# Kernel tuning notes

Hardware: AMD Instinct MI355X
Metric: run time of the kernel (lower is better)

## Reference

```python
import jax, jax.numpy as jnp
import numpy as np

INPUT_DIM = 362
HIDDEN = 256
STYLE_NUM = 60
OUTFIT_NUM = 49710
BATCH = 16384


def setup_inputs() -> dict:
    key = jax.random.key(0)
    ks = jax.random.split(key, 12)
    f32 = jnp.float32
    return {
        "i_feature": jax.random.normal(ks[0], (BATCH, INPUT_DIM), f32),
        "j_feature": jax.random.normal(ks[1], (BATCH, INPUT_DIM), f32),
        "k_feature": jax.random.normal(ks[2], (BATCH, INPUT_DIM), f32),
        # top_emb / bottom_emb Linear params (stored transposed: x @ W + b)
        "W_top": jax.random.normal(ks[3], (INPUT_DIM, HIDDEN), f32) * 0.05,
        "b_top": jnp.zeros((HIDDEN,), f32),
        "W_bot": jax.random.normal(ks[4], (INPUT_DIM, HIDDEN), f32) * 0.05,
        "b_bot": jnp.zeros((HIDDEN,), f32),
        # NMF factors (forward relu_'s them in place; we relu on use)
        "P_nmf": jax.random.normal(ks[5], (2 * INPUT_DIM, STYLE_NUM), f32),
        "N_nmf": jax.random.normal(ks[6], (2 * INPUT_DIM, STYLE_NUM), f32),
        "H1_nmf": jax.random.normal(ks[7], (STYLE_NUM, OUTFIT_NUM), f32),
        "H2_nmf": jax.random.normal(ks[8], (STYLE_NUM, OUTFIT_NUM), f32),
        "matirx_pos": jax.random.uniform(ks[9], (2 * INPUT_DIM, OUTFIT_NUM), f32),
        "matirx_neg": jax.random.uniform(ks[10], (2 * INPUT_DIM, OUTFIT_NUM), f32),
    }


def _emb(x, W, b):
    # nn.Sequential(Linear, Sigmoid)
    return jax.nn.sigmoid(x @ W + b)


def _style_score(i_f, j_f, styles, W_top, b_top, W_bot, b_bot):
    # Vectorized version of the per-sample loop:
    # squared-distance argmin codebook lookup + gather + rowwise dot.
    outfit = jnp.concatenate([i_f, j_f], axis=1)  # [B, 2D]
    # mean over feature dim of (x - s)^2; constant 1/(2D) scale does not change argmin
    d2 = (jnp.sum(outfit * outfit, axis=1, keepdims=True)
          - 2.0 * (outfit @ styles)
          + jnp.sum(styles * styles, axis=0, keepdims=True))  # [B, S]
    idx = jnp.argmin(d2, axis=1)                               # [B]
    sel = styles.T[idx]                                        # [B, 2D] gather
    top, bot = sel[:, :INPUT_DIM], sel[:, INPUT_DIM:]
    # diag(matmul) == rowwise dot
    return jnp.sum(_emb(top, W_top, b_top) * _emb(bot, W_bot, b_bot), axis=1)  # [B]


def reference(i_feature, j_feature, k_feature, W_top, b_top, W_bot, b_bot,
              P_nmf, N_nmf, H1_nmf, H2_nmf, matirx_pos, matirx_neg):
    Ti = _emb(i_feature, W_top, b_top)   # [B, H]
    Bj = _emb(j_feature, W_bot, b_bot)   # [B, H]
    Bk = _emb(k_feature, W_bot, b_bot)   # [B, H]
    # torch.diag(matmul(Ti, Bj.T)) == rowwise dot (avoids [B,B] intermediate)
    ij_score = jnp.sum(Ti * Bj, axis=1)  # [B]
    ik_score = jnp.sum(Ti * Bk, axis=1)  # [B]

    # forward does relu_ on .data before use
    P = jnp.maximum(P_nmf, 0.0)
    N = jnp.maximum(N_nmf, 0.0)
    H1 = jnp.maximum(H1_nmf, 0.0)
    H2 = jnp.maximum(H2_nmf, 0.0)

    style_ij = _style_score(i_feature, j_feature, P, W_top, b_top, W_bot, b_bot)
    style_ik = _style_score(i_feature, k_feature, N, W_top, b_top, W_bot, b_bot)

    # -mean(log(sigmoid(d))) computed stably
    loss1 = -jnp.mean(jax.nn.log_sigmoid(ij_score - ik_score))
    loss2 = -jnp.mean(jax.nn.log_sigmoid(style_ij - style_ik))
    loss3 = jnp.mean(jnp.square(matirx_pos - P @ H1)
                     + jnp.square(matirx_neg - N @ H2))
    loss = loss1 + loss2 + 0.1 * loss3

    ij_ik = jnp.stack([ij_score, ik_score], axis=1)  # [B, 2]
    auc = jnp.mean((jnp.argmax(ij_ik, axis=1) == 0).astype(jnp.float32))
    return (loss, loss1, loss2, loss3, auc)
```

## Files before the change

### kernel.cpp

```cpp
#include <hip/hip_runtime.h>
#include <math.h>

#define BATCH 16384
#define IND   362
#define KP    384
#define HID   256
#define STY   60
#define NOUT  49710
#define OUTP  49920
#define D2    724
#define D2P   768

#define NB_HR   3120
#define NB_CW   768
#define NB_CPN  384
#define NB_CF   9216
#define NB_CONV (NB_HR + NB_CW + NB_CPN + NB_CF)

#define NB_SS   120

#define OCH     256
#define N_OC    195
#define DHALF   368
#define NTILES  23
#define NB_M    (2 * 2 * N_OC)

#define NB_EMB  1024
#define NB_SA   512
#define NB_HH   16
#define NB_PPB  2
#define NB_HEAD (NB_HH + NB_PPB)

typedef __bf16 bf16x8 __attribute__((ext_vector_type(8)));
typedef float  floatx4 __attribute__((ext_vector_type(4)));
typedef float  floatx2 __attribute__((ext_vector_type(2)));

__device__ inline floatx4 mfma16(bf16x8 a, bf16x8 b, floatx4 c) {
  return __builtin_amdgcn_mfma_f32_16x16x32_bf16(a, b, c, 0, 0, 0);
}

__device__ inline unsigned short f32_to_bf16(float x) {
  unsigned int u = __float_as_uint(x);
  unsigned int r = (u + 0x7FFFu + ((u >> 16) & 1u)) >> 16;
  return (unsigned short)r;
}

__device__ inline float sigm_fast(float x) { return 1.0f / (1.0f + __expf(-x)); }
__device__ inline float softplusf(float z) { return fmaxf(z, 0.0f) + log1pf(expf(-fabsf(z))); }

__global__ __launch_bounds__(256) void k_conv(
    const float* __restrict__ fi, const float* __restrict__ fj, const float* __restrict__ fk,
    const float* __restrict__ Wt, const float* __restrict__ Wb,
    const float* __restrict__ Pn, const float* __restrict__ Nn,
    const float* __restrict__ H1, const float* __restrict__ H2,
    unsigned short* __restrict__ fbf, unsigned short* __restrict__ wbfT,
    unsigned short* __restrict__ pnbfT, unsigned short* __restrict__ hrows,
    float* __restrict__ Pr) {
  int b = blockIdx.x;
  int t = threadIdx.x;

  if (b < NB_HR) {
    int e = (b * 256 + t) * 8;
    int row = e / OUTP;
    int o = e - row * OUTP;
    int s = row & 63;
    int mm = row >> 6;
    const float* H = mm ? H2 : H1;
    unsigned short* dst = hrows + (size_t)row * OUTP + o;
    unsigned int wv[4];
    if (s < STY && o + 8 <= NOUT) {
      const float* src = H + (size_t)s * NOUT + o;
      #pragma unroll
      for (int ee = 0; ee < 4; ee++) {
        floatx2 v = *(const floatx2*)(src + 2 * ee);
        wv[ee] = (unsigned)f32_to_bf16(fmaxf(v[0], 0.0f)) |
                 ((unsigned)f32_to_bf16(fmaxf(v[1], 0.0f)) << 16);
      }
    } else {
      #pragma unroll
      for (int ee = 0; ee < 4; ee++) {
        float lo = (s < STY && o + 2 * ee     < NOUT) ? fmaxf(H[(size_t)s * NOUT + o + 2 * ee],     0.0f) : 0.0f;
        float hi = (s < STY && o + 2 * ee + 1 < NOUT) ? fmaxf(H[(size_t)s * NOUT + o + 2 * ee + 1], 0.0f) : 0.0f;
        wv[ee] = (unsigned)f32_to_bf16(lo) | ((unsigned)f32_to_bf16(hi) << 16);
      }
    }
    uint4 v; v.x = wv[0]; v.y = wv[1]; v.z = wv[2]; v.w = wv[3];
    *(uint4*)dst = v;
    return;
  }
  b -= NB_HR;

  if (b < NB_CW) {
    int idx = b * 256 + t;
    int k = idx % KP;
    int rem = idx / KP;
    int h = rem % HID;
    int mm = rem / HID;
    const float* W = mm ? Wb : Wt;
    wbfT[idx] = f32_to_bf16(k < IND ? W[(size_t)k * HID + h] : 0.0f);
    return;
  }
  b -= NB_CW;

  if (b < NB_CPN) {
    int u = b * 256 + t;
    int s = u & 63;
    int v = u >> 6;
    int m = (v >= D2P) ? 1 : 0;
    int d = v - m * D2P;
    const float* M = m ? Nn : Pn;
    float x = (d < D2 && s < STY) ? fmaxf(M[(size_t)d * STY + s], 0.0f) : 0.0f;
    unsigned short bb = f32_to_bf16(x);
    int k = (d < IND) ? d : (d < D2 ? d + 22 : (d < 746 ? d - IND : d));
    pnbfT[((size_t)m * 64 + s) * D2P + k] = bb;
    Pr[((size_t)m * D2P + d) * 64 + s] = x;
    return;
  }
  b -= NB_CPN;

  {
    long u = (long)b * 256 + t;
    int g = (int)(u % 48);
    long rf = u / 48;
    int row = (int)(rf % BATCH);
    int f = (int)(rf / BATCH);
    const float* src = (f == 0) ? fi : (f == 1 ? fj : fk);
    int d0 = g * 8;
    const float* sp = src + (size_t)row * IND + d0;
    unsigned int wv[4];
    #pragma unroll
    for (int e = 0; e < 4; e++) {
      int dd = d0 + 2 * e;
      float lo = (dd < IND)     ? sp[2 * e]     : 0.0f;
      float hi = (dd + 1 < IND) ? sp[2 * e + 1] : 0.0f;
      wv[e] = (unsigned)f32_to_bf16(lo) | ((unsigned)f32_to_bf16(hi) << 16);
    }
    uint4 v; v.x = wv[0]; v.y = wv[1]; v.z = wv[2]; v.w = wv[3];
    *(uint4*)(fbf + ((size_t)f * BATCH + row) * KP + d0) = v;
  }
}

__global__ __launch_bounds__(256) void k_style(
    const float* __restrict__ Wt, const float* __restrict__ btop,
    const float* __restrict__ Wb, const float* __restrict__ bbot,
    const float* __restrict__ Pn, const float* __restrict__ Nn,
    float* __restrict__ ss, float* __restrict__ cn) {
  __shared__ float sel[D2];
  __shared__ float shr[4];
  int b = blockIdx.x;
  int t = threadIdx.x;
  int s  = b % STY;
  int mt = b / STY;
  const float* M = mt ? Nn : Pn;
  float cnp = 0.0f;
  for (int d = t; d < D2; d += 256) {
    float v = fmaxf(M[(size_t)d * STY + s], 0.0f);
    sel[d] = v;
    cnp += v * v;
  }
  __syncthreads();
  float at = btop[t], ab = bbot[t];
  for (int d = 0; d < IND; d++) at = fmaf(sel[d],       Wt[(size_t)d * HID + t], at);
  for (int d = 0; d < IND; d++) ab = fmaf(sel[IND + d], Wb[(size_t)d * HID + t], ab);
  float prod = (1.0f / (1.0f + expf(-at))) * (1.0f / (1.0f + expf(-ab)));
  for (int off = 32; off > 0; off >>= 1) prod += __shfl_xor(prod, off);
  if ((t & 63) == 0) shr[t >> 6] = prod;
  __syncthreads();
  if (t == 0) ss[mt * 64 + s] = shr[0] + shr[1] + shr[2] + shr[3];
  __syncthreads();
  for (int off = 32; off > 0; off >>= 1) cnp += __shfl_xor(cnp, off);
  if ((t & 63) == 0) shr[t >> 6] = cnp;
  __syncthreads();
  if (t == 0) cn[mt * 64 + s] = shr[0] + shr[1] + shr[2] + shr[3];
}

__global__ __launch_bounds__(256) void k_m(
    const unsigned short* __restrict__ hrows, const float* __restrict__ Pr,
    const float* __restrict__ mp, const float* __restrict__ mneg,
    float* __restrict__ partial) {
  __shared__ unsigned short Hs[64 * OCH];
  __shared__ float red[4];
  int w = threadIdx.x >> 6, lane = threadIdx.x & 63;
  int m = lane & 15, q = lane >> 4;

  int b = blockIdx.x;
  int oc  = b % N_OC;
  int r   = b / N_OC;
  int dh  = r & 1;
  int mat = r >> 1;
  int o0 = oc * OCH;
  bool full = (o0 + OCH <= NOUT);
  const float* Mbase = mat ? mneg : mp;
  const float* Prb   = Pr + (size_t)mat * D2P * 64;

  char* HsB = (char*)Hs;
  #pragma unroll
  for (int rr = 0; rr < 16; rr++) {
    int R = w * 16 + rr;
    uint2 hv = *(const uint2*)(hrows + ((size_t)mat * 64 + R) * OUTP + o0 + lane * 4);
    *(uint2*)(HsB + R * 512 + ((lane * 8) ^ ((R & 7) << 4))) = hv;
  }
  __syncthreads();

  int xm = (m & 7) << 4;
  float msq = 0.0f, t2 = 0.0f;
  floatx2 mreg[32];
  floatx4 preg[4];

  auto ISSUE_M = [&](int t) {
    int d = dh * DHALF + t * 16 + m;
    bool ok = (d < D2);
    const float* Mr = Mbase + (size_t)d * NOUT + o0 + q * 8;
    if (ok && full) {
      #pragma unroll
      for (int kc = 0; kc < 8; kc++) {
        mreg[kc * 4 + 0] = *(const floatx2*)(Mr + kc * 32);
        mreg[kc * 4 + 1] = *(const floatx2*)(Mr + kc * 32 + 2);
        mreg[kc * 4 + 2] = *(const floatx2*)(Mr + kc * 32 + 4);
        mreg[kc * 4 + 3] = *(const floatx2*)(Mr + kc * 32 + 6);
      }
    } else {
      #pragma unroll
      for (int kc = 0; kc < 8; kc++) {
        #pragma unroll
        for (int e = 0; e < 4; e++) {
          int o = o0 + kc * 32 + q * 8 + 2 * e;
          floatx2 v = {0.f, 0.f};
          if (ok) {
            if (o     < NOUT) v[0] = Mbase[(size_t)d * NOUT + o];
            if (o + 1 < NOUT) v[1] = Mbase[(size_t)d * NOUT + o + 1];
          }
          mreg[kc * 4 + e] = v;
        }
      }
    }
  };
  auto ISSUE_P = [&](int t) {
    int d = dh * DHALF + t * 16 + m;
    const float* Pp = Prb + (size_t)d * 64 + q * 4;
    #pragma unroll
    for (int st = 0; st < 4; st++) preg[st] = *(const floatx4*)(Pp + st * 16);
  };

  int t0 = w;
  if (t0 < NTILES) { ISSUE_M(t0); ISSUE_P(t0); }
  for (int t = t0; t < NTILES; t += 4) {
    bf16x8 bf[8];
    #pragma unroll
    for (int kc = 0; kc < 8; kc++) {
      union { unsigned int u[4]; bf16x8 v; } cv;
      #pragma unroll
      for (int e = 0; e < 4; e++) {
        floatx2 tv = mreg[kc * 4 + e];
        msq = fmaf(tv[0], tv[0], msq);
        msq = fmaf(tv[1], tv[1], msq);
        cv.u[e] = (unsigned)f32_to_bf16(tv[0]) | ((unsigned)f32_to_bf16(tv[1]) << 16);
      }
      bf[kc] = cv.v;
    }
    int tn = t + 4;
    if (tn < NTILES) ISSUE_M(tn);

    floatx4 acc[4];
    #pragma unroll
    for (int st = 0; st < 4; st++) acc[st] = (floatx4){0.f, 0.f, 0.f, 0.f};
    #pragma unroll
    for (int kc = 0; kc < 8; kc++) {
      #pragma unroll
      for (int st = 0; st < 4; st++) {
        bf16x8 hf = *(const bf16x8*)(HsB + (st * 16 + m) * 512 + ((kc * 64 + q * 16) ^ xm));
        acc[st] = mfma16(hf, bf[kc], acc[st]);
      }
    }

    #pragma unroll
    for (int st = 0; st < 4; st++)
      #pragma unroll
      for (int rg = 0; rg < 4; rg++)
        t2 = fmaf(preg[st][rg], acc[st][rg], t2);
    if (tn < NTILES) ISSUE_P(tn);
  }

  float local = msq - 2.0f * t2;
  for (int off = 32; off > 0; off >>= 1) local += __shfl_xor(local, off);
  if (lane == 0) red[w] = local;
  __syncthreads();
  if (threadIdx.x == 0) partial[blockIdx.x] = red[0] + red[1] + red[2] + red[3];
}

__global__ __launch_bounds__(256, 4) void k_emb(
    const unsigned short* __restrict__ fbf, const unsigned short* __restrict__ wbfT,
    const float* __restrict__ btop, const float* __restrict__ bbot,
    float* __restrict__ sIJ, float* __restrict__ sIK) {
  int w = threadIdx.x >> 6, lane = threadIdx.x & 63;
  int m = lane & 15, q = lane >> 4;
  int b = blockIdx.x;
  int r0 = (b & 255) * 64 + w * 16;
  int hb = (b >> 8) * 64;
  const unsigned short* fi = fbf + (size_t)(r0 + m) * KP + q * 8;
  const unsigned short* fj = fi + (size_t)BATCH * KP;
  const unsigned short* fk = fj + (size_t)BATCH * KP;
  floatx4 accI[4], accJ[4], accK[4];
  #pragma unroll
  for (int nt = 0; nt < 4; nt++) {
    accI[nt] = (floatx4){0.f, 0.f, 0.f, 0.f};
    accJ[nt] = (floatx4){0.f, 0.f, 0.f, 0.f};
    accK[nt] = (floatx4){0.f, 0.f, 0.f, 0.f};
  }
  for (int kc = 0; kc < 12; kc++) {
    bf16x8 ai = *(const bf16x8*)(fi + kc * 32);
    bf16x8 aj = *(const bf16x8*)(fj + kc * 32);
    bf16x8 ak = *(const bf16x8*)(fk + kc * 32);
    #pragma unroll
    for (int nt = 0; nt < 4; nt++) {
      int n = hb + nt * 16 + m;
      const unsigned short* wp = wbfT + (size_t)n * KP + kc * 32 + q * 8;
      bf16x8 bt8 = *(const bf16x8*)(wp);
      bf16x8 bb8 = *(const bf16x8*)(wp + (size_t)HID * KP);
      accI[nt] = mfma16(ai, bt8, accI[nt]);
      accJ[nt] = mfma16(aj, bb8, accJ[nt]);
      accK[nt] = mfma16(ak, bb8, accK[nt]);
    }
  }
  float sij[4] = {0.f, 0.f, 0.f, 0.f}, sik[4] = {0.f, 0.f, 0.f, 0.f};
  #pragma unroll
  for (int nt = 0; nt < 4; nt++) {
    int n = hb + nt * 16 + m;
    float vbt = btop[n], vbb = bbot[n];
    #pragma unroll
    for (int reg = 0; reg < 4; reg++) {
      float ti = sigm_fast(accI[nt][reg] + vbt);
      float tj = sigm_fast(accJ[nt][reg] + vbb);
      float tk = sigm_fast(accK[nt][reg] + vbb);
      sij[reg] += ti * tj;
      sik[reg] += ti * tk;
    }
  }
  #pragma unroll
  for (int reg = 0; reg < 4; reg++) {
    for (int off = 1; off < 16; off <<= 1) {
      sij[reg] += __shfl_xor(sij[reg], off);
      sik[reg] += __shfl_xor(sik[reg], off);
    }
  }
  if (m == 0) {
    #pragma unroll
    for (int reg = 0; reg < 4; reg++) {
      int row = r0 + q * 4 + reg;
      atomicAdd(&sIJ[row], sij[reg]);
      atomicAdd(&sIK[row], sik[reg]);
    }
  }
}

__global__ __launch_bounds__(256, 4) void k_sa(
    const unsigned short* __restrict__ fbf, const unsigned short* __restrict__ pnbfT,
    const float* __restrict__ cn, const float* __restrict__ ss,
    float* __restrict__ stIJ, float* __restrict__ stIK) {
  int w = threadIdx.x >> 6, lane = threadIdx.x & 63;
  int m = lane & 15, q = lane >> 4;
  int b = blockIdx.x;
  int mat = w & 1;
  int r0 = b * 32 + (w >> 1) * 16;
  const unsigned short* fA = fbf + (size_t)(r0 + m) * KP + q * 8;
  const unsigned short* fB = fA + (size_t)(1 + mat) * BATCH * KP;
  const unsigned short* Bp = pnbfT + (size_t)mat * 64 * D2P + q * 8;
  floatx4 acc[4];
  #pragma unroll
  for (int nt = 0; nt < 4; nt++) acc[nt] = (floatx4){0.f, 0.f, 0.f, 0.f};
  for (int kc = 0; kc < 24; kc++) {
    bf16x8 a = (kc < 12) ? *(const bf16x8*)(fA + kc * 32)
                         : *(const bf16x8*)(fB + (kc - 12) * 32);
    #pragma unroll
    for (int nt = 0; nt < 4; nt++) {
      bf16x8 bb = *(const bf16x8*)(Bp + (size_t)(nt * 16 + m) * D2P + kc * 32);
      acc[nt] = mfma16(a, bb, acc[nt]);
    }
  }
  const float* cnm = cn + mat * 64;
  float bv[4]; int bi[4];
  #pragma unroll
  for (int reg = 0; reg < 4; reg++) { bv[reg] = __builtin_inff(); bi[reg] = 1 << 30; }
  #pragma unroll
  for (int nt = 0; nt < 4; nt++) {
    int s = nt * 16 + m;
    float c = cnm[s & 63];
    #pragma unroll
    for (int reg = 0; reg < 4; reg++) {
      float d2 = (s < STY) ? (c - 2.0f * acc[nt][reg]) : __builtin_inff();
      if (d2 < bv[reg] || (d2 == bv[reg] && s < bi[reg])) { bv[reg] = d2; bi[reg] = s; }
    }
  }
  for (int off = 1; off < 16; off <<= 1) {
    #pragma unroll
    for (int reg = 0; reg < 4; reg++) {
      float ov = __shfl_xor(bv[reg], off);
      int   oi = __shfl_xor(bi[reg], off);
      if (ov < bv[reg] || (ov == bv[reg] && oi < bi[reg])) { bv[reg] = ov; bi[reg] = oi; }
    }
  }
  if (m == 0) {
    float* dst = mat ? stIK : stIJ;
    const float* ssm = ss + mat * 64;
    #pragma unroll
    for (int reg = 0; reg < 4; reg++) dst[r0 + q * 4 + reg] = ssm[bi[reg]];
  }
}

__global__ __launch_bounds__(256) void k_head(
    const unsigned short* __restrict__ pnbfT, const unsigned short* __restrict__ hrows,
    float* __restrict__ HHb, float* __restrict__ PPb) {
  __shared__ float red[4096];
  int w = threadIdx.x >> 6, lane = threadIdx.x & 63;
  int m = lane & 15, q = lane >> 4;
  int b = blockIdx.x;
  bool isPP = (b >= NB_HH);
  int mat, chunk, nsteps, stride;
  const unsigned short* Rb;
  if (!isPP) { mat = b >> 3; chunk = b & 7; Rb = hrows + (size_t)mat * 64 * OUTP; stride = OUTP; nsteps = 195; }
  else       { mat = b - NB_HH; chunk = 0; Rb = pnbfT + (size_t)mat * 64 * D2P;  stride = D2P;  nsteps = 24;  }
  const unsigned short* Rm = Rb + (size_t)m * stride;

  floatx4 acc[4][4];
  #pragma unroll
  for (int a2 = 0; a2 < 4; a2++)
    #pragma unroll
    for (int b2 = 0; b2 < 4; b2++) acc[a2][b2] = (floatx4){0.f, 0.f, 0.f, 0.f};

  bf16x8 hc[4], hn[4];
  auto LD = [&](int j, bf16x8* hh) {
    int k = (chunk * nsteps + j) * 32 + q * 8;
    #pragma unroll
    for (int st = 0; st < 4; st++)
      hh[st] = *(const bf16x8*)(Rm + (size_t)(st * 16) * stride + k);
  };
  int j = w;
  LD(j, hc);
  for (; j < nsteps; j += 4) {
    if (j + 4 < nsteps) LD(j + 4, hn);
    #pragma unroll
    for (int a2 = 0; a2 < 4; a2++)
      #pragma unroll
      for (int b2 = 0; b2 < 4; b2++)
        acc[a2][b2] = mfma16(hc[a2], hc[b2], acc[a2][b2]);
    #pragma unroll
    for (int st = 0; st < 4; st++) hc[st] = hn[st];
  }
  for (int idx = threadIdx.x; idx < 4096; idx += 256) red[idx] = 0.f;
  __syncthreads();
  #pragma unroll
  for (int a2 = 0; a2 < 4; a2++)
    #pragma unroll
    for (int b2 = 0; b2 < 4; b2++)
      #pragma unroll
      for (int r = 0; r < 4; r++)
        atomicAdd(&red[(a2 * 16 + q * 4 + r) * 64 + b2 * 16 + m], acc[a2][b2][r]);
  __syncthreads();
  float* dst = (isPP ? PPb : HHb) + (size_t)mat * 4096;
  for (int idx = threadIdx.x; idx < 4096; idx += 256) atomicAdd(&dst[idx], red[idx]);
}

__global__ __launch_bounds__(256) void k_final(
    const float* __restrict__ sIJ, const float* __restrict__ sIK,
    const float* __restrict__ stIJ, const float* __restrict__ stIK,
    const float* __restrict__ l3partial,
    const float* __restrict__ HHb, const float* __restrict__ PPb,
    float* __restrict__ out) {
  int t = threadIdx.x;
  float l1 = 0.f, l2 = 0.f, ac = 0.f;
  for (int r = t; r < BATCH; r += 256) {
    float dij = sIJ[r] - sIK[r];
    l1 += softplusf(-dij);
    if (dij >= 0.0f) ac += 1.0f;
    float dst = stIJ[r] - stIK[r];
    l2 += softplusf(-dst);
  }
  double l3 = 0.0;
  for (int p = t; p < NB_M; p += 256) l3 += (double)l3partial[p];
  for (int idx = t; idx < 8192; idx += 256) l3 += (double)HHb[idx] * (double)PPb[idx];
  __shared__ float sh1[4], sh2[4], sh3[4];
  __shared__ double sh4[4];
  for (int off = 32; off > 0; off >>= 1) {
    l1 += __shfl_xor(l1, off);
    l2 += __shfl_xor(l2, off);
    ac += __shfl_xor(ac, off);
    l3 += __shfl_xor(l3, off);
  }
  if ((t & 63) == 0) { sh1[t >> 6] = l1; sh2[t >> 6] = l2; sh3[t >> 6] = ac; sh4[t >> 6] = l3; }
  __syncthreads();
  if (t == 0) {
    double L1 = 0, L2 = 0, AC = 0, L3 = 0;
    for (int i = 0; i < 4; i++) { L1 += sh1[i]; L2 += sh2[i]; AC += sh3[i]; L3 += sh4[i]; }
    L1 /= BATCH; L2 /= BATCH; AC /= BATCH;
    L3 /= ((double)D2 * (double)NOUT);
    out[0] = (float)(L1 + L2 + 0.1 * L3);
    out[1] = (float)L1;
    out[2] = (float)L2;
    out[3] = (float)L3;
    out[4] = (float)AC;
  }
}

extern "C" void kernel_launch(void* const* d_in, const int* in_sizes, int n_in,
                              void* d_out, int out_size, void* d_ws, size_t ws_size,
                              hipStream_t stream) {
  (void)in_sizes; (void)n_in; (void)out_size; (void)ws_size;
  const float* i_f  = (const float*)d_in[0];
  const float* j_f  = (const float*)d_in[1];
  const float* k_f  = (const float*)d_in[2];
  const float* W_t  = (const float*)d_in[3];
  const float* b_t  = (const float*)d_in[4];
  const float* W_b  = (const float*)d_in[5];
  const float* b_b  = (const float*)d_in[6];
  const float* P_n  = (const float*)d_in[7];
  const float* N_n  = (const float*)d_in[8];
  const float* H1   = (const float*)d_in[9];
  const float* H2   = (const float*)d_in[10];
  const float* Mp   = (const float*)d_in[11];
  const float* Mn   = (const float*)d_in[12];
  float* out = (float*)d_out;
  char* ws = (char*)d_ws;

  const size_t OFF_FBF   = 0;
  const size_t OFF_WBFT  = OFF_FBF   + (size_t)3 * BATCH * KP * 2;
  const size_t OFF_PNBFT = OFF_WBFT  + (size_t)2 * HID * KP * 2;
  const size_t OFF_PR    = OFF_PNBFT + (size_t)2 * 64 * D2P * 2;
  const size_t OFF_HROWS = OFF_PR    + (size_t)2 * D2P * 64 * 4;
  const size_t OFF_SIJ   = OFF_HROWS + (size_t)2 * 64 * OUTP * 2;
  const size_t OFF_SIK   = OFF_SIJ   + (size_t)BATCH * 4;
  const size_t OFF_HH    = OFF_SIK   + (size_t)BATCH * 4;
  const size_t OFF_PP    = OFF_HH    + (size_t)2 * 4096 * 4;
  const size_t OFF_STIJ  = OFF_PP    + (size_t)2 * 4096 * 4;
  const size_t OFF_STIK  = OFF_STIJ  + (size_t)BATCH * 4;
  const size_t OFF_SS    = OFF_STIK  + (size_t)BATCH * 4;
  const size_t OFF_CN    = OFF_SS    + 512;
  const size_t OFF_L3P   = OFF_CN    + 512;

  unsigned short* fbf   = (unsigned short*)(ws + OFF_FBF);
  unsigned short* wbfT  = (unsigned short*)(ws + OFF_WBFT);
  unsigned short* pnbfT = (unsigned short*)(ws + OFF_PNBFT);
  float*          Pr    = (float*)(ws + OFF_PR);
  unsigned short* hrows = (unsigned short*)(ws + OFF_HROWS);
  float*  sIJ  = (float*)(ws + OFF_SIJ);
  float*  sIK  = (float*)(ws + OFF_SIK);
  float*  HHb  = (float*)(ws + OFF_HH);
  float*  PPb  = (float*)(ws + OFF_PP);
  float*  stIJ = (float*)(ws + OFF_STIJ);
  float*  stIK = (float*)(ws + OFF_STIK);
  float*  ss   = (float*)(ws + OFF_SS);
  float*  cn   = (float*)(ws + OFF_CN);
  float*  l3p  = (float*)(ws + OFF_L3P);

  hipMemsetAsync(ws + OFF_SIJ, 0, (size_t)BATCH * 4 * 2 + (size_t)4 * 4096 * 4, stream);

  k_conv<<<NB_CONV, 256, 0, stream>>>(i_f, j_f, k_f, W_t, W_b, P_n, N_n, H1, H2,
                                      fbf, wbfT, pnbfT, hrows, Pr);
  k_style<<<NB_SS, 256, 0, stream>>>(W_t, b_t, W_b, b_b, P_n, N_n, ss, cn);
  k_m<<<NB_M, 256, 0, stream>>>(hrows, Pr, Mp, Mn, l3p);
  k_emb<<<NB_EMB, 256, 0, stream>>>(fbf, wbfT, b_t, b_b, sIJ, sIK);
  k_sa<<<NB_SA, 256, 0, stream>>>(fbf, pnbfT, cn, ss, stIJ, stIK);
  k_head<<<NB_HEAD, 256, 0, stream>>>(pnbfT, hrows, HHb, PPb);
  k_final<<<1, 256, 0, stream>>>(sIJ, sIK, stIJ, stIK, l3p, HHb, PPb, out);
}
```

Baseline: 698.6 us.

## Fuse M, embedding, style-assign and head kernels into one launch; restage M tiles via LDS

Merges the four independent compute kernels (NMF residual, embedding scores, style argmin, Gram heads) into a single block-dispatched kernel, so their work can overlap on the GPU and fewer launches are needed. The NMF residual path is rewritten to load matrix rows coalesced into registers, convert them to bf16 into double-buffered swizzled shared memory, and run one MFMA chain per wave, with a barrier each tile. The final reduction is split into a 64-block partial kernel plus a small finalize kernel, and index arithmetic in the conversion kernel moves from 64-bit to 32-bit. The fused kernel now reserves about 48KB of shared memory for every block, which can lower occupancy for the embedding and style-assign blocks that previously used none.

```diff
diff --git a/kernel.cpp b/kernel.cpp
--- a/kernel.cpp
+++ b/kernel.cpp
@@ -22,14 +22,14 @@
 #define OCH     256
 #define N_OC    195
 #define DHALF   368
-#define NTILES  23
-#define NB_M    (2 * 2 * N_OC)
-
+#define MTILES  23
+#define NB_MB   (2 * 2 * N_OC)
 #define NB_EMB  1024
 #define NB_SA   512
 #define NB_HH   16
 #define NB_PPB  2
 #define NB_HEAD (NB_HH + NB_PPB)
+#define NB_MAIN (NB_MB + NB_EMB + NB_SA + NB_HEAD)
 
 typedef __bf16 bf16x8 __attribute__((ext_vector_type(8)));
 typedef float  floatx4 __attribute__((ext_vector_type(4)));
@@ -119,11 +119,11 @@
   b -= NB_CPN;
 
   {
-    long u = (long)b * 256 + t;
-    int g = (int)(u % 48);
-    long rf = u / 48;
-    int row = (int)(rf % BATCH);
-    int f = (int)(rf / BATCH);
+    int u = b * 256 + t;
+    int g = u % 48;
+    int rf = u / 48;
+    int row = rf % BATCH;
+    int f = rf / BATCH;
     const float* src = (f == 0) ? fi : (f == 1 ? fj : fk);
     int d0 = g * 8;
     const float* sp = src + (size_t)row * IND + d0;
@@ -174,309 +174,301 @@
   if (t == 0) cn[mt * 64 + s] = shr[0] + shr[1] + shr[2] + shr[3];
 }
 
-__global__ __launch_bounds__(256) void k_m(
-    const unsigned short* __restrict__ hrows, const float* __restrict__ Pr,
+__global__ __launch_bounds__(256) void k_main(
+    const unsigned short* __restrict__ fbf, const unsigned short* __restrict__ wbfT,
+    const unsigned short* __restrict__ pnbfT, const unsigned short* __restrict__ hrows,
+    const float* __restrict__ Pr,
+    const float* __restrict__ btop, const float* __restrict__ bbot,
+    const float* __restrict__ cn, const float* __restrict__ ss,
     const float* __restrict__ mp, const float* __restrict__ mneg,
+    float* __restrict__ sIJ, float* __restrict__ sIK,
+    float* __restrict__ stIJ, float* __restrict__ stIK,
+    float* __restrict__ HHb, float* __restrict__ PPb,
     float* __restrict__ partial) {
-  __shared__ unsigned short Hs[64 * OCH];
-  __shared__ float red[4];
-  int w = threadIdx.x >> 6, lane = threadIdx.x & 63;
-  int m = lane & 15, q = lane >> 4;
-
-  int b = blockIdx.x;
-  int oc  = b % N_OC;
-  int r   = b / N_OC;
-  int dh  = r & 1;
-  int mat = r >> 1;
-  int o0 = oc * OCH;
-  bool full = (o0 + OCH <= NOUT);
-  const float* Mbase = mat ? mneg : mp;
-  const float* Prb   = Pr + (size_t)mat * D2P * 64;
-
-  char* HsB = (char*)Hs;
-  #pragma unroll
-  for (int rr = 0; rr < 16; rr++) {
-    int R = w * 16 + rr;
-    uint2 hv = *(const uint2*)(hrows + ((size_t)mat * 64 + R) * OUTP + o0 + lane * 4);
-    *(uint2*)(HsB + R * 512 + ((lane * 8) ^ ((R & 7) << 4))) = hv;
-  }
-  __syncthreads();
-
-  int xm = (m & 7) << 4;
-  float msq = 0.0f, t2 = 0.0f;
-  floatx2 mreg[32];
-  floatx4 preg[4];
-
-  auto ISSUE_M = [&](int t) {
-    int d = dh * DHALF + t * 16 + m;
-    bool ok = (d < D2);
-    const float* Mr = Mbase + (size_t)d * NOUT + o0 + q * 8;
-    if (ok && full) {
-      #pragma unroll
-      for (int kc = 0; kc < 8; kc++) {
-        mreg[kc * 4 + 0] = *(const floatx2*)(Mr + kc * 32);
-        mreg[kc * 4 + 1] = *(const floatx2*)(Mr + kc * 32 + 2);
-        mreg[kc * 4 + 2] = *(const floatx2*)(Mr + kc * 32 + 4);
-        mreg[kc * 4 + 3] = *(const floatx2*)(Mr + kc * 32 + 6);
-      }
-    } else {
-      #pragma unroll
-      for (int kc = 0; kc < 8; kc++) {
-        #pragma unroll
-        for (int e = 0; e < 4; e++) {
-          int o = o0 + kc * 32 + q * 8 + 2 * e;
-          floatx2 v = {0.f, 0.f};
-          if (ok) {
-            if (o     < NOUT) v[0] = Mbase[(size_t)d * NOUT + o];
-            if (o + 1 < NOUT) v[1] = Mbase[(size_t)d * NOUT + o + 1];
-          }
-          mreg[kc * 4 + e] = v;
-        }
-      }
-    }
-  };
-  auto ISSUE_P = [&](int t) {
-    int d = dh * DHALF + t * 16 + m;
-    const float* Pp = Prb + (size_t)d * 64 + q * 4;
-    #pragma unroll
-    for (int st = 0; st < 4; st++) preg[st] = *(const floatx4*)(Pp + st * 16);
-  };
-
-  int t0 = w;
-  if (t0 < NTILES) { ISSUE_M(t0); ISSUE_P(t0); }
-  for (int t = t0; t < NTILES; t += 4) {
-    bf16x8 bf[8];
-    #pragma unroll
-    for (int kc = 0; kc < 8; kc++) {
-      union { unsigned int u[4]; bf16x8 v; } cv;
-      #pragma unroll
-      for (int e = 0; e < 4; e++) {
-        floatx2 tv = mreg[kc * 4 + e];
-        msq = fmaf(tv[0], tv[0], msq);
-        msq = fmaf(tv[1], tv[1], msq);
-        cv.u[e] = (unsigned)f32_to_bf16(tv[0]) | ((unsigned)f32_to_bf16(tv[1]) << 16);
-      }
-      bf[kc] = cv.v;
-    }
-    int tn = t + 4;
-    if (tn < NTILES) ISSUE_M(tn);
-
-    floatx4 acc[4];
-    #pragma unroll
-    for (int st = 0; st < 4; st++) acc[st] = (floatx4){0.f, 0.f, 0.f, 0.f};
-    #pragma unroll
-    for (int kc = 0; kc < 8; kc++) {
-      #pragma unroll
-      for (int st = 0; st < 4; st++) {
-        bf16x8 hf = *(const bf16x8*)(HsB + (st * 16 + m) * 512 + ((kc * 64 + q * 16) ^ xm));
-        acc[st] = mfma16(hf, bf[kc], acc[st]);
-      }
-    }
-
-    #pragma unroll
-    for (int st = 0; st < 4; st++)
-      #pragma unroll
-      for (int rg = 0; rg < 4; rg++)
-        t2 = fmaf(preg[st][rg], acc[st][rg], t2);
-    if (tn < NTILES) ISSUE_P(tn);
-  }
-
-  float local = msq - 2.0f * t2;
-  for (int off = 32; off > 0; off >>= 1) local += __shfl_xor(local, off);
-  if (lane == 0) red[w] = local;
-  __syncthreads();
-  if (threadIdx.x == 0) partial[blockIdx.x] = red[0] + red[1] + red[2] + red[3];
-}
-
-__global__ __launch_bounds__(256, 4) void k_emb(
-    const unsigned short* __restrict__ fbf, const unsigned short* __restrict__ wbfT,
-    const float* __restrict__ btop, const float* __restrict__ bbot,
-    float* __restrict__ sIJ, float* __restrict__ sIK) {
+  __shared__ __align__(16) char smem[49168];
   int w = threadIdx.x >> 6, lane = threadIdx.x & 63;
   int m = lane & 15, q = lane >> 4;
   int b = blockIdx.x;
-  int r0 = (b & 255) * 64 + w * 16;
-  int hb = (b >> 8) * 64;
-  const unsigned short* fi = fbf + (size_t)(r0 + m) * KP + q * 8;
-  const unsigned short* fj = fi + (size_t)BATCH * KP;
-  const unsigned short* fk = fj + (size_t)BATCH * KP;
-  floatx4 accI[4], accJ[4], accK[4];
-  #pragma unroll
-  for (int nt = 0; nt < 4; nt++) {
-    accI[nt] = (floatx4){0.f, 0.f, 0.f, 0.f};
-    accJ[nt] = (floatx4){0.f, 0.f, 0.f, 0.f};
-    accK[nt] = (floatx4){0.f, 0.f, 0.f, 0.f};
-  }
-  for (int kc = 0; kc < 12; kc++) {
-    bf16x8 ai = *(const bf16x8*)(fi + kc * 32);
-    bf16x8 aj = *(const bf16x8*)(fj + kc * 32);
-    bf16x8 ak = *(const bf16x8*)(fk + kc * 32);
+
+  if (b < NB_MB) {
+    int oc  = b % N_OC;
+    int r   = b / N_OC;
+    int dh  = r & 1;
+    int mat = r >> 1;
+    int o0 = oc * OCH;
+    int nvalid = NOUT - o0; if (nvalid > OCH) nvalid = OCH;
+    const float* Mbase = mat ? mneg : mp;
+    const float* Prb   = Pr + (size_t)mat * D2P * 64;
+    char* HsB = smem;
+    char* MsB = smem + 32768;
+    float* shp = (float*)(smem + 49152);
+
+    #pragma unroll
+    for (int rr = 0; rr < 16; rr++) {
+      int R = w * 16 + rr;
+      uint2 hv = *(const uint2*)(hrows + ((size_t)mat * 64 + R) * OUTP + o0 + lane * 4);
+      *(uint2*)(HsB + R * 512 + ((lane * 8) ^ ((R & 7) << 4))) = hv;
+    }
+
+    float msq = 0.0f, t2 = 0.0f;
+    float rgA[4][4], rgB[4][4];
+
+    auto ISSUE = [&](int t, float rg[4][4]) {
+      #pragma unroll
+      for (int rr = 0; rr < 4; rr++) {
+        int row = w * 4 + rr;
+        int d = dh * DHALF + t * 16 + row;
+        bool ok = (d < D2);
+        const float* src = Mbase + (size_t)d * NOUT + o0;
+        #pragma unroll
+        for (int e = 0; e < 4; e++) {
+          int c = lane + 64 * e;
+          rg[rr][e] = (ok && c < nvalid) ? src[c] : 0.0f;
+        }
+      }
+    };
+    auto WRITE = [&](int t, float rg[4][4]) {
+      char* buf = MsB + (t & 1) * 8192;
+      #pragma unroll
+      for (int rr = 0; rr < 4; rr++) {
+        int row = w * 4 + rr;
+        int swz = (row & 7) << 4;
+        #pragma unroll
+        for (int e = 0; e < 4; e++) {
+          float v = rg[rr][e];
+          msq = fmaf(v, v, msq);
+          *(unsigned short*)(buf + row * 512 + (((lane + 64 * e) * 2) ^ swz)) = f32_to_bf16(v);
+        }
+      }
+    };
+
+    ISSUE(0, rgA);
+    ISSUE(1, rgB);
+    WRITE(0, rgA);
+    __syncthreads();
+
+    int xm = (m & 7) << 4;
+    for (int t = 0; t < MTILES; t++) {
+      if (t + 2 < MTILES) ISSUE(t + 2, (t & 1) ? rgB : rgA);
+      int dbase = dh * DHALF + t * 16;
+      floatx4 pv = *(const floatx4*)(Prb + (size_t)(dbase + m) * 64 + w * 16 + q * 4);
+      const char* buf = MsB + (t & 1) * 8192;
+      floatx4 acc = (floatx4){0.f, 0.f, 0.f, 0.f};
+      #pragma unroll
+      for (int kc = 0; kc < 8; kc++) {
+        bf16x8 hf = *(const bf16x8*)(HsB + (w * 16 + m) * 512 + ((kc * 64 + q * 16) ^ xm));
+        bf16x8 mf = *(const bf16x8*)(buf + m * 512 + ((kc * 64 + q * 16) ^ xm));
+        acc = mfma16(hf, mf, acc);
+      }
+      if (t + 1 < MTILES) WRITE(t + 1, (t & 1) ? rgA : rgB);
+      t2 = fmaf(pv[0], acc[0], fmaf(pv[1], acc[1], fmaf(pv[2], acc[2], fmaf(pv[3], acc[3], t2))));
+      __syncthreads();
+    }
+
+    float local = msq - 2.0f * t2;
+    for (int off = 32; off > 0; off >>= 1) local += __shfl_xor(local, off);
+    if (lane == 0) shp[w] = local;
+    __syncthreads();
+    if (threadIdx.x == 0) partial[blockIdx.x] = shp[0] + shp[1] + shp[2] + shp[3];
+    return;
+  }
+  b -= NB_MB;
+
+  if (b < NB_EMB) {
+    int r0 = (b & 255) * 64 + w * 16;
+    int hb = (b >> 8) * 64;
+    const unsigned short* fi = fbf + (size_t)(r0 + m) * KP + q * 8;
+    const unsigned short* fj = fi + (size_t)BATCH * KP;
+    const unsigned short* fk = fj + (size_t)BATCH * KP;
+    floatx4 accI[4], accJ[4], accK[4];
+    #pragma unroll
+    for (int nt = 0; nt < 4; nt++) {
+      accI[nt] = (floatx4){0.f, 0.f, 0.f, 0.f};
+      accJ[nt] = (floatx4){0.f, 0.f, 0.f, 0.f};
+      accK[nt] = (floatx4){0.f, 0.f, 0.f, 0.f};
+    }
+    for (int kc = 0; kc < 12; kc++) {
+      bf16x8 ai = *(const bf16x8*)(fi + kc * 32);
+      bf16x8 aj = *(const bf16x8*)(fj + kc * 32);
+      bf16x8 ak = *(const bf16x8*)(fk + kc * 32);
+      #pragma unroll
+      for (int nt = 0; nt < 4; nt++) {
+        int n = hb + nt * 16 + m;
+        const unsigned short* wp = wbfT + (size_t)n * KP + kc * 32 + q * 8;
+        bf16x8 bt8 = *(const bf16x8*)(wp);
+        bf16x8 bb8 = *(const bf16x8*)(wp + (size_t)HID * KP);
+        accI[nt] = mfma16(ai, bt8, accI[nt]);
+        accJ[nt] = mfma16(aj, bb8, accJ[nt]);
+        accK[nt] = mfma16(ak, bb8, accK[nt]);
+      }
+    }
+    float sij[4] = {0.f, 0.f, 0.f, 0.f}, sik[4] = {0.f, 0.f, 0.f, 0.f};
     #pragma unroll
     for (int nt = 0; nt < 4; nt++) {
       int n = hb + nt * 16 + m;
-      const unsigned short* wp = wbfT + (size_t)n * KP + kc * 32 + q * 8;
-      bf16x8 bt8 = *(const bf16x8*)(wp);
-      bf16x8 bb8 = *(const bf16x8*)(wp + (size_t)HID * KP);
-      accI[nt] = mfma16(ai, bt8, accI[nt]);
-      accJ[nt] = mfma16(aj, bb8, accJ[nt]);
-      accK[nt] = mfma16(ak, bb8, accK[nt]);
-    }
-  }
-  float sij[4] = {0.f, 0.f, 0.f, 0.f}, sik[4] = {0.f, 0.f, 0.f, 0.f};
-  #pragma unroll
-  for (int nt = 0; nt < 4; nt++) {
-    int n = hb + nt * 16 + m;
-    float vbt = btop[n], vbb = bbot[n];
+      float vbt = btop[n], vbb = bbot[n];
+      #pragma unroll
+      for (int reg = 0; reg < 4; reg++) {
+        float ti = sigm_fast(accI[nt][reg] + vbt);
+        float tj = sigm_fast(accJ[nt][reg] + vbb);
+        float tk = sigm_fast(accK[nt][reg] + vbb);
+        sij[reg] += ti * tj;
+        sik[reg] += ti * tk;
+      }
+    }
     #pragma unroll
     for (int reg = 0; reg < 4; reg++) {
-      float ti = sigm_fast(accI[nt][reg] + vbt);
-      float tj = sigm_fast(accJ[nt][reg] + vbb);
-      float tk = sigm_fast(accK[nt][reg] + vbb);
-      sij[reg] += ti * tj;
-      sik[reg] += ti * tk;
-    }
-  }
-  #pragma unroll
-  for (int reg = 0; reg < 4; reg++) {
+      for (int off = 1; off < 16; off <<= 1) {
+        sij[reg] += __shfl_xor(sij[reg], off);
+        sik[reg] += __shfl_xor(sik[reg], off);
+      }
+    }
+    if (m == 0) {
+      #pragma unroll
+      for (int reg = 0; reg < 4; reg++) {
+        int row = r0 + q * 4 + reg;
+        atomicAdd(&sIJ[row], sij[reg]);
+        atomicAdd(&sIK[row], sik[reg]);
+      }
+    }
+    return;
+  }
+  b -= NB_EMB;
+
+  if (b < NB_SA) {
+    int mat = w & 1;
+    int r0 = b * 32 + (w >> 1) * 16;
+    const unsigned short* fA = fbf + (size_t)(r0 + m) * KP + q * 8;
+    const unsigned short* fB = fA + (size_t)(1 + mat) * BATCH * KP;
+    const unsigned short* Bp = pnbfT + (size_t)mat * 64 * D2P + q * 8;
+    floatx4 acc[4];
+    #pragma unroll
+    for (int nt = 0; nt < 4; nt++) acc[nt] = (floatx4){0.f, 0.f, 0.f, 0.f};
+    for (int kc = 0; kc < 24; kc++) {
+      bf16x8 a = (kc < 12) ? *(const bf16x8*)(fA + kc * 32)
+                           : *(const bf16x8*)(fB + (kc - 12) * 32);
+      #pragma unroll
+      for (int nt = 0; nt < 4; nt++) {
+        bf16x8 bb = *(const bf16x8*)(Bp + (size_t)(nt * 16 + m) * D2P + kc * 32);
+        acc[nt] = mfma16(a, bb, acc[nt]);
+      }
+    }
+    const float* cnm = cn + mat * 64;
+    float bv[4]; int bi[4];
+    #pragma unroll
+    for (int reg = 0; reg < 4; reg++) { bv[reg] = __builtin_inff(); bi[reg] = 1 << 30; }
+    #pragma unroll
+    for (int nt = 0; nt < 4; nt++) {
+      int s = nt * 16 + m;
+      float c = cnm[s & 63];
+      #pragma unroll
+      for (int reg = 0; reg < 4; reg++) {
+        float d2 = (s < STY) ? (c - 2.0f * acc[nt][reg]) : __builtin_inff();
+        if (d2 < bv[reg] || (d2 == bv[reg] && s < bi[reg])) { bv[reg] = d2; bi[reg] = s; }
+      }
+    }
     for (int off = 1; off < 16; off <<= 1) {
-      sij[reg] += __shfl_xor(sij[reg], off);
-      sik[reg] += __shfl_xor(sik[reg], off);
-    }
-  }
-  if (m == 0) {
-    #pragma unroll
-    for (int reg = 0; reg < 4; reg++) {
-      int row = r0 + q * 4 + reg;
-      atomicAdd(&sIJ[row], sij[reg]);
-      atomicAdd(&sIK[row], sik[reg]);
-    }
-  }
-}
-
-__global__ __launch_bounds__(256, 4) void k_sa(
-    const unsigned short* __restrict__ fbf, const unsigned short* __restrict__ pnbfT,
-    const float* __restrict__ cn, const float* __restrict__ ss,
-    float* __restrict__ stIJ, float* __restrict__ stIK) {
-  int w = threadIdx.x >> 6, lane = threadIdx.x & 63;
-  int m = lane & 15, q = lane >> 4;
-  int b = blockIdx.x;
-  int mat = w & 1;
-  int r0 = b * 32 + (w >> 1) * 16;
-  const unsigned short* fA = fbf + (size_t)(r0 + m) * KP + q * 8;
-  const unsigned short* fB = fA + (size_t)(1 + mat) * BATCH * KP;
-  const unsigned short* Bp = pnbfT + (size_t)mat * 64 * D2P + q * 8;
-  floatx4 acc[4];
-  #pragma unroll
-  for (int nt = 0; nt < 4; nt++) acc[nt] = (floatx4){0.f, 0.f, 0.f, 0.f};
-  for (int kc = 0; kc < 24; kc++) {
-    bf16x8 a = (kc < 12) ? *(const bf16x8*)(fA + kc * 32)
-                         : *(const bf16x8*)(fB + (kc - 12) * 32);
-    #pragma unroll
-    for (int nt = 0; nt < 4; nt++) {
-      bf16x8 bb = *(const bf16x8*)(Bp + (size_t)(nt * 16 + m) * D2P + kc * 32);
-      acc[nt] = mfma16(a, bb, acc[nt]);
-    }
-  }
-  const float* cnm = cn + mat * 64;
-  float bv[4]; int bi[4];
-  #pragma unroll
-  for (int reg = 0; reg < 4; reg++) { bv[reg] = __builtin_inff(); bi[reg] = 1 << 30; }
-  #pragma unroll
-  for (int nt = 0; nt < 4; nt++) {
-    int s = nt * 16 + m;
-    float c = cnm[s & 63];
-    #pragma unroll
-    for (int reg = 0; reg < 4; reg++) {
-      float d2 = (s < STY) ? (c - 2.0f * acc[nt][reg]) : __builtin_inff();
-      if (d2 < bv[reg] || (d2 == bv[reg] && s < bi[reg])) { bv[reg] = d2; bi[reg] = s; }
-    }
-  }
-  for (int off = 1; off < 16; off <<= 1) {
-    #pragma unroll
-    for (int reg = 0; reg < 4; reg++) {
-      float ov = __shfl_xor(bv[reg], off);
-      int   oi = __shfl_xor(bi[reg], off);
-      if (ov < bv[reg] || (ov == bv[reg] && oi < bi[reg])) { bv[reg] = ov; bi[reg] = oi; }
-    }
-  }
-  if (m == 0) {
-    float* dst = mat ? stIK : stIJ;
-    const float* ssm = ss + mat * 64;
-    #pragma unroll
-    for (int reg = 0; reg < 4; reg++) dst[r0 + q * 4 + reg] = ssm[bi[reg]];
-  }
-}
-
-__global__ __launch_bounds__(256) void k_head(
-    const unsigned short* __restrict__ pnbfT, const unsigned short* __restrict__ hrows,
-    float* __restrict__ HHb, float* __restrict__ PPb) {
-  __shared__ float red[4096];
-  int w = threadIdx.x >> 6, lane = threadIdx.x & 63;
-  int m = lane & 15, q = lane >> 4;
-  int b = blockIdx.x;
-  bool isPP = (b >= NB_HH);
-  int mat, chunk, nsteps, stride;
-  const unsigned short* Rb;
-  if (!isPP) { mat = b >> 3; chunk = b & 7; Rb = hrows + (size_t)mat * 64 * OUTP; stride = OUTP; nsteps = 195; }
-  else       { mat = b - NB_HH; chunk = 0; Rb = pnbfT + (size_t)mat * 64 * D2P;  stride = D2P;  nsteps = 24;  }
-  const unsigned short* Rm = Rb + (size_t)m * stride;
-
-  floatx4 acc[4][4];
-  #pragma unroll
-  for (int a2 = 0; a2 < 4; a2++)
-    #pragma unroll
-    for (int b2 = 0; b2 < 4; b2++) acc[a2][b2] = (floatx4){0.f, 0.f, 0.f, 0.f};
-
-  bf16x8 hc[4], hn[4];
-  auto LD = [&](int j, bf16x8* hh) {
-    int k = (chunk * nsteps + j) * 32 + q * 8;
-    #pragma unroll
-    for (int st = 0; st < 4; st++)
-      hh[st] = *(const bf16x8*)(Rm + (size_t)(st * 16) * stride + k);
-  };
-  int j = w;
-  LD(j, hc);
-  for (; j < nsteps; j += 4) {
-    if (j + 4 < nsteps) LD(j + 4, hn);
+      #pragma unroll
+      for (int reg = 0; reg < 4; reg++) {
+        float ov = __shfl_xor(bv[reg], off);
+        int   oi = __shfl_xor(bi[reg], off);
+        if (ov < bv[reg] || (ov == bv[reg] && oi < bi[reg])) { bv[reg] = ov; bi[reg] = oi; }
+      }
+    }
+    if (m == 0) {
+      float* dst = mat ? stIK : stIJ;
+      const float* ssm = ss + mat * 64;
+      #pragma unroll
+      for (int reg = 0; reg < 4; reg++) dst[r0 + q * 4 + reg] = ssm[bi[reg]];
+    }
+    return;
+  }
+  b -= NB_SA;
+
+  {
+    float* red = (float*)smem;
+    bool isPP = (b >= NB_HH);
+    int mat, chunk, nsteps, stride;
+    const unsigned short* Rb;
+    if (!isPP) { mat = b >> 3; chunk = b & 7; Rb = hrows + (size_t)mat * 64 * OUTP; stride = OUTP; nsteps = 195; }
+    else       { mat = b - NB_HH; chunk = 0; Rb = pnbfT + (size_t)mat * 64 * D2P;  stride = D2P;  nsteps = 24;  }
+    const unsigned short* Rm = Rb + (size_t)m * stride;
+
+    floatx4 acc[4][4];
     #pragma unroll
     for (int a2 = 0; a2 < 4; a2++)
       #pragma unroll
+      for (int b2 = 0; b2 < 4; b2++) acc[a2][b2] = (floatx4){0.f, 0.f, 0.f, 0.f};
+
+    bf16x8 hc[4], hn[4];
+    auto LD = [&](int j, bf16x8* hh) {
+      int k = (chunk * nsteps + j) * 32 + q * 8;
+      #pragma unroll
+      for (int st = 0; st < 4; st++)
+        hh[st] = *(const bf16x8*)(Rm + (size_t)(st * 16) * stride + k);
+    };
+    int j = w;
+    LD(j, hc);
+    for (; j < nsteps; j += 4) {
+      if (j + 4 < nsteps) LD(j + 4, hn);
+      #pragma unroll
+      for (int a2 = 0; a2 < 4; a2++)
+        #pragma unroll
+        for (int b2 = 0; b2 < 4; b2++)
+          acc[a2][b2] = mfma16(hc[a2], hc[b2], acc[a2][b2]);
+      #pragma unroll
+      for (int st = 0; st < 4; st++) hc[st] = hn[st];
+    }
+    for (int idx = threadIdx.x; idx < 4096; idx += 256) red[idx] = 0.f;
+    __syncthreads();
+    #pragma unroll
+    for (int a2 = 0; a2 < 4; a2++)
+      #pragma unroll
       for (int b2 = 0; b2 < 4; b2++)
-        acc[a2][b2] = mfma16(hc[a2], hc[b2], acc[a2][b2]);
-    #pragma unroll
-    for (int st = 0; st < 4; st++) hc[st] = hn[st];
-  }
-  for (int idx = threadIdx.x; idx < 4096; idx += 256) red[idx] = 0.f;
-  __syncthreads();
-  #pragma unroll
-  for (int a2 = 0; a2 < 4; a2++)
-    #pragma unroll
-    for (int b2 = 0; b2 < 4; b2++)
-      #pragma unroll
-      for (int r = 0; r < 4; r++)
-        atomicAdd(&red[(a2 * 16 + q * 4 + r) * 64 + b2 * 16 + m], acc[a2][b2][r]);
-  __syncthreads();
-  float* dst = (isPP ? PPb : HHb) + (size_t)mat * 4096;
-  for (int idx = threadIdx.x; idx < 4096; idx += 256) atomicAdd(&dst[idx], red[idx]);
-}
-
-__global__ __launch_bounds__(256) void k_final(
+        #pragma unroll
+        for (int r = 0; r < 4; r++)
+          atomicAdd(&red[(a2 * 16 + q * 4 + r) * 64 + b2 * 16 + m], acc[a2][b2][r]);
+    __syncthreads();
+    float* dst = (isPP ? PPb : HHb) + (size_t)mat * 4096;
+    for (int idx = threadIdx.x; idx < 4096; idx += 256) atomicAdd(&dst[idx], red[idx]);
+  }
+}
+
+__global__ __launch_bounds__(256) void k_red(
     const float* __restrict__ sIJ, const float* __restrict__ sIK,
     const float* __restrict__ stIJ, const float* __restrict__ stIK,
-    const float* __restrict__ l3partial,
+    float* __restrict__ red5) {
+  __shared__ float sh[3][4];
+  int t = threadIdx.x;
+  int r = blockIdx.x * 256 + t;
+  float dij = sIJ[r] - sIK[r];
+  float l1 = softplusf(-dij);
+  float ac = (dij >= 0.0f) ? 1.0f : 0.0f;
+  float dst = stIJ[r] - stIK[r];
+  float l2 = softplusf(-dst);
+  for (int off = 32; off > 0; off >>= 1) {
+    l1 += __shfl_xor(l1, off);
+    l2 += __shfl_xor(l2, off);
+    ac += __shfl_xor(ac, off);
+  }
+  if ((t & 63) == 0) { sh[0][t >> 6] = l1; sh[1][t >> 6] = l2; sh[2][t >> 6] = ac; }
+  __syncthreads();
+  if (t == 0) {
+    red5[blockIdx.x * 4 + 0] = sh[0][0] + sh[0][1] + sh[0][2] + sh[0][3];
+    red5[blockIdx.x * 4 + 1] = sh[1][0] + sh[1][1] + sh[1][2] + sh[1][3];
+    red5[blockIdx.x * 4 + 2] = sh[2][0] + sh[2][1] + sh[2][2] + sh[2][3];
+  }
+}
+
+__global__ __launch_bounds__(256) void k_fin(
+    const float* __restrict__ red5, const float* __restrict__ l3partial,
     const float* __restrict__ HHb, const float* __restrict__ PPb,
     float* __restrict__ out) {
   int t = threadIdx.x;
   float l1 = 0.f, l2 = 0.f, ac = 0.f;
-  for (int r = t; r < BATCH; r += 256) {
-    float dij = sIJ[r] - sIK[r];
-    l1 += softplusf(-dij);
-    if (dij >= 0.0f) ac += 1.0f;
-    float dst = stIJ[r] - stIK[r];
-    l2 += softplusf(-dst);
-  }
+  if (t < 64) { l1 = red5[t * 4]; l2 = red5[t * 4 + 1]; ac = red5[t * 4 + 2]; }
   double l3 = 0.0;
-  for (int p = t; p < NB_M; p += 256) l3 += (double)l3partial[p];
+  for (int p = t; p < NB_MB; p += 256) l3 += (double)l3partial[p];
   for (int idx = t; idx < 8192; idx += 256) l3 += (double)HHb[idx] * (double)PPb[idx];
   __shared__ float sh1[4], sh2[4], sh3[4];
   __shared__ double sh4[4];
@@ -535,6 +527,7 @@
   const size_t OFF_SS    = OFF_STIK  + (size_t)BATCH * 4;
   const size_t OFF_CN    = OFF_SS    + 512;
   const size_t OFF_L3P   = OFF_CN    + 512;
+  const size_t OFF_RED5  = OFF_L3P   + 4096;
 
   unsigned short* fbf   = (unsigned short*)(ws + OFF_FBF);
   unsigned short* wbfT  = (unsigned short*)(ws + OFF_WBFT);
@@ -550,15 +543,16 @@
   float*  ss   = (float*)(ws + OFF_SS);
   float*  cn   = (float*)(ws + OFF_CN);
   float*  l3p  = (float*)(ws + OFF_L3P);
+  float*  red5 = (float*)(ws + OFF_RED5);
 
   hipMemsetAsync(ws + OFF_SIJ, 0, (size_t)BATCH * 4 * 2 + (size_t)4 * 4096 * 4, stream);
 
   k_conv<<<NB_CONV, 256, 0, stream>>>(i_f, j_f, k_f, W_t, W_b, P_n, N_n, H1, H2,
                                       fbf, wbfT, pnbfT, hrows, Pr);
   k_style<<<NB_SS, 256, 0, stream>>>(W_t, b_t, W_b, b_b, P_n, N_n, ss, cn);
-  k_m<<<NB_M, 256, 0, stream>>>(hrows, Pr, Mp, Mn, l3p);
-  k_emb<<<NB_EMB, 256, 0, stream>>>(fbf, wbfT, b_t, b_b, sIJ, sIK);
-  k_sa<<<NB_SA, 256, 0, stream>>>(fbf, pnbfT, cn, ss, stIJ, stIK);
-  k_head<<<NB_HEAD, 256, 0, stream>>>(pnbfT, hrows, HHb, PPb);
-  k_final<<<1, 256, 0, stream>>>(sIJ, sIK, stIJ, stIK, l3p, HHb, PPb, out);
-}
+  k_main<<<NB_MAIN, 256, 0, stream>>>(fbf, wbfT, pnbfT, hrows, Pr,
+                                      b_t, b_b, cn, ss, Mp, Mn,
+                                      sIJ, sIK, stIJ, stIK, HHb, PPb, l3p);
+  k_red<<<BATCH / 256, 256, 0, stream>>>(sIJ, sIK, stIJ, stIK, red5);
+  k_fin<<<1, 256, 0, stream>>>(red5, l3p, HHb, PPb, out);
+}
```

Measured after the change: 728.6 us. 1.04x slower.
